# Kernel optimization log

Measured on AMD Instinct MI355X. Metric: run time of the kernel, lower is better.

Reference implementation:

```python
import jax, jax.numpy as jnp
import numpy as np

N, M, H, C = 20000, 20000, 32, 128
KP_EXTENT = 0.6
EPS = 1e-5


def _kpconv(q_pts, s_pts, neighb_inds, x, kernel_points, weights):
    """Rigid KPConv, linear influence, 'sum' aggregation, Predator-style density norm."""
    # shadow point / shadow feature padding (index M is the shadow slot)
    s_pad = jnp.concatenate([s_pts, jnp.full((1, 3), 1e6, s_pts.dtype)], axis=0)
    x_pad = jnp.concatenate([x, jnp.zeros((1, x.shape[1]), x.dtype)], axis=0)
    neighbors = s_pad[neighb_inds] - q_pts[:, None, :]              # [N,H,3]
    diff = neighbors[:, :, None, :] - kernel_points[None, None]      # [N,H,K,3]
    sq = jnp.sum(diff * diff, axis=-1)                               # [N,H,K]
    dist = jnp.sqrt(jnp.maximum(sq, 1e-12))
    all_weights = jnp.clip(1.0 - dist / KP_EXTENT, 0.0, None)        # linear KP influence
    neighb_x = x_pad[neighb_inds]                                    # [N,H,C]
    weighted = jnp.einsum('nhk,nhc->nkc', all_weights, neighb_x)     # [N,K,C]
    out = jnp.einsum('nkc,kcd->nd', weighted, weights)               # [N,D]
    # density normalization by number of valid neighbors
    feat_sum = jnp.sum(neighb_x, axis=-1)                            # [N,H]
    n_num = jnp.maximum(jnp.sum(feat_sum > 0.0, axis=-1), 1)         # [N]
    return out / n_num[:, None].astype(out.dtype)


def _segment_norm(x, len0):
    """Per-cloud (instance) normalization over stacked points, 2 clouds, no affine."""
    n = x.shape[0]
    seg = (jnp.arange(n) >= len0).astype(jnp.int32)                  # [N] in {0,1}
    onehot = jax.nn.one_hot(seg, 2, dtype=x.dtype)                   # [N,2]
    cnt = jnp.maximum(onehot.sum(axis=0), 1.0)                       # [2]
    mean = (onehot.T @ x) / cnt[:, None]                             # [2,C]
    var = (onehot.T @ (x * x)) / cnt[:, None] - mean * mean          # [2,C]
    return (x - mean[seg]) * jax.lax.rsqrt(var[seg] + EPS)


def _batchnorm1d(x, gamma, beta):
    mean = jnp.mean(x, axis=0)
    var = jnp.mean(x * x, axis=0) - mean * mean                      # biased, as torch BN
    return (x - mean) * jax.lax.rsqrt(var + EPS) * gamma + beta


def _rand_kernel_points(key, k, radius):
    pts = jax.random.normal(key, (k, 3), dtype=jnp.float32)
    pts = pts / jnp.linalg.norm(pts, axis=1, keepdims=True)
    r = jax.random.uniform(jax.random.fold_in(key, 1), (k, 1)) ** (1.0 / 3.0)
    return pts * r * radius


def setup_inputs() -> dict:
    key = jax.random.key(0)
    ks = jax.random.split(key, 10)
    D = C // 2  # 64, per-branch out channels
    q_pts = jax.random.uniform(ks[0], (N, 3), dtype=jnp.float32)
    s_pts = jax.random.uniform(ks[1], (M, 3), dtype=jnp.float32)
    neighb_inds = jax.random.randint(ks[2], (N, H), 0, M)
    x = jax.random.normal(ks[3], (M, C), dtype=jnp.float32)
    stack_lengths_post = jnp.array([N // 2, N - N // 2], dtype=jnp.int32)
    kp_mini = _rand_kernel_points(ks[4], 7, 1.0 * 1.5)               # radius * 1.5
    w_mini = jax.random.normal(ks[5], (7, C, D), dtype=jnp.float32) * (1.0 / np.sqrt(C))
    kp_mid = _rand_kernel_points(ks[6], 13, 1.0)                      # radius
    w_mid = jax.random.normal(ks[7], (13, C, D), dtype=jnp.float32) * (1.0 / np.sqrt(C))
    w_midmini = jax.random.normal(ks[8], (D, D), dtype=jnp.float32) * (1.0 / np.sqrt(D))
    w_final = jax.random.normal(ks[9], (C, C), dtype=jnp.float32) * (1.0 / np.sqrt(C))
    gamma_final = jnp.ones((C,), jnp.float32)
    beta_final = jnp.zeros((C,), jnp.float32)
    return dict(q_pts=q_pts, s_pts=s_pts, neighb_inds=neighb_inds, x=x,
                stack_lengths_post=stack_lengths_post,
                kp_mini=kp_mini, w_mini=w_mini, kp_mid=kp_mid, w_mid=w_mid,
                w_midmini=w_midmini, w_final=w_final,
                gamma_final=gamma_final, beta_final=beta_final)


def reference(q_pts, s_pts, neighb_inds, x, stack_lengths_post,
              kp_mini, w_mini, kp_mid, w_mid, w_midmini, w_final,
              gamma_final, beta_final):
    len0 = stack_lengths_post[0]
    x1 = _kpconv(q_pts, s_pts, neighb_inds, x, kp_mini, w_mini)      # [N, C//2]
    x1 = _segment_norm(x1, len0)
    x2 = _kpconv(q_pts, s_pts, neighb_inds, x, kp_mid, w_mid)        # [N, C//2]
    x2 = _segment_norm(x2, len0)
    x2 = (x1 + x2) @ w_midmini.T                                     # nn.Linear(bias=False)
    xc = jnp.concatenate([x1, x2], axis=1)                           # [N, C]
    out = xc @ w_final.T
    out = _batchnorm1d(out, gamma_final, beta_final)
    return jax.nn.relu(out)
```

## Files before the change

kernel.cpp:

```cpp
#include <hip/hip_runtime.h>
#include <math.h>

#define NQ 20000
#define MS 20000
#define HN 32
#define CH 128
#define DH 64
#define KTOT 20
#define KMINI 7
#define EPSN 1e-5f
#define NKT 80
#define KT_Y1 28

#define OFF_ROWSUM 0
#define OFF_Y1     20480
#define OFF_Y2     (OFF_Y1 + NQ*DH)
#define OFF_SEGSUM (OFF_Y2 + NQ*DH)
#define OFF_BNSUM  (OFF_SEGSUM + 512)
#define OFF_BNSQ   (OFF_BNSUM + 128)
#define OFF_OUTPRE (OFF_BNSQ + 128)
#define OFF_WSWZ   (OFF_OUTPRE + NQ*CH)
#define OFF_CFRAG  (OFF_WSWZ + 163840)
#define OFF_XBF    (OFF_CFRAG + 8192)
#define TOT_FLOATS (OFF_XBF + NQ*CH/2)

#define PK 40
#define PQ 840

typedef __attribute__((ext_vector_type(8))) short bf16x8;
typedef __attribute__((ext_vector_type(4))) float f32x4;
typedef __attribute__((ext_vector_type(4))) unsigned short us4;
typedef __attribute__((ext_vector_type(8))) unsigned short us8;

static __device__ inline unsigned short f2bf(float f) {
    unsigned int u = __float_as_uint(f);
    unsigned int r = (u + 0x7fffu + ((u >> 16) & 1u)) >> 16;
    return (unsigned short)r;
}

__global__ __launch_bounds__(256) void k_prep(
    const float* __restrict__ x, float* __restrict__ rowsum,
    const float* __restrict__ w_mini, const float* __restrict__ w_mid,
    const float* __restrict__ w_midmini, const float* __restrict__ w_final,
    unsigned short* __restrict__ wswz, unsigned short* __restrict__ cfrag,
    unsigned short* __restrict__ x_bf)
{
    const int t = threadIdx.x;
    if (blockIdx.x < 1250) {
        int row = blockIdx.x * 16 + (t >> 4);
        int l16 = t & 15;
        const float4* xr = (const float4*)&x[(size_t)row * CH + l16 * 8];
        float4 a = xr[0], b = xr[1];
        if (x_bf) {
            us8 v;
            v[0] = f2bf(a.x); v[1] = f2bf(a.y); v[2] = f2bf(a.z); v[3] = f2bf(a.w);
            v[4] = f2bf(b.x); v[5] = f2bf(b.y); v[6] = f2bf(b.z); v[7] = f2bf(b.w);
            *(us8*)&x_bf[(size_t)row * CH + l16 * 8] = v;
        }
        double s = (double)a.x + a.y + a.z + a.w + b.x + b.y + b.z + b.w;
        #pragma unroll
        for (int off = 8; off > 0; off >>= 1) s += __shfl_down(s, off, 64);
        if (l16 == 0) rowsum[row] = (float)s;
    } else if (blockIdx.x < 2530) {
        int gid = (blockIdx.x - 1250) * 256 + t;
        if (gid >= NKT * 8 * 512) return;
        int j = gid & 7;
        int l = (gid >> 3) & 63;
        int ntkt = gid >> 9;
        int nt = ntkt & 7;
        int kt = ntkt >> 3;
        int kg = kt * 32 + ((l >> 4) << 3) + j;
        int d  = nt * 16 + (l & 15);
        int k = kg >> 7, c = kg & 127;
        float v = 0.0f;
        if (k < KMINI && d < DH)        v = w_mini[((size_t)k * CH + c) * DH + d];
        else if (k >= KMINI && d >= DH) v = w_mid[((size_t)(k - KMINI) * CH + c) * DH + (d - DH)];
        wswz[gid] = f2bf(v);
    } else {
        int b2 = blockIdx.x - 2530;
        int kt = b2 >> 3, nt = b2 & 7;
        for (int e = t; e < 512; e += 256) {
            int l = e >> 3, j = e & 7;
            int i = kt * 32 + ((l >> 4) << 3) + j;
            int jcol = nt * 16 + (l & 15);
            const float* wfr = &w_final[(size_t)jcol * 128 + 64];
            int ec = i & 63;
            float dsum = 0.f;
            #pragma unroll 8
            for (int dd = 0; dd < 64; ++dd)
                dsum += w_midmini[dd * 64 + ec] * wfr[dd];
            float cv = dsum + ((i < 64) ? w_final[(size_t)jcol * 128 + i] : 0.f);
            cfrag[(size_t)(kt * 8 + nt) * 512 + e] = f2bf(cv);
        }
    }
}

__global__ __launch_bounds__(256) void k_fused2(
    const float* __restrict__ q_pts, const float* __restrict__ s_pts,
    const int* __restrict__ inds, const unsigned short* __restrict__ x_bf,
    const float* __restrict__ kp_mini, const float* __restrict__ kp_mid,
    const float* __restrict__ rowsum, const unsigned short* __restrict__ wswz,
    const int* __restrict__ stacklen,
    float* __restrict__ y1, float* __restrict__ y2, float* __restrict__ segsum)
{
    __shared__ __align__(16) char pool[36096];
    unsigned short* Pt = (unsigned short*)pool;
    unsigned short* xg = (unsigned short*)(pool + 26880);
    float* nbv = (float*)pool;
    __shared__ int nidx[512];
    __shared__ float kpts[KTOT][3];
    __shared__ int vcnt[16];
    __shared__ float winv[16];

    const int t = threadIdx.x;
    const int l = t & 63;
    const int w = t >> 6;
    const int c16 = l & 15;
    const int quad = l >> 4;
    const int n0 = blockIdx.x * 16;

    if (t < KTOT * 3) {
        int k = t / 3, j = t % 3;
        kpts[k][j] = (k < KMINI) ? kp_mini[k * 3 + j] : kp_mid[(k - KMINI) * 3 + j];
    }
    if (t < 16) vcnt[t] = 0;
    __syncthreads();

    for (int tt = t; tt < 512; tt += 256) {
        int r = tt >> 5, h = tt & 31;
        int n = n0 + r;
        int idx = inds[n * HN + h];
        nidx[tt] = idx;
        float qx = q_pts[n * 3 + 0], qy = q_pts[n * 3 + 1], qz = q_pts[n * 3 + 2];
        nbv[tt * 3 + 0] = s_pts[idx * 3 + 0] - qx;
        nbv[tt * 3 + 1] = s_pts[idx * 3 + 1] - qy;
        nbv[tt * 3 + 2] = s_pts[idx * 3 + 2] - qz;
        if (rowsum[idx] > 0.0f) atomicAdd(&vcnt[r], 1);
    }
    __syncthreads();
    if (t < 16) winv[t] = 1.0f / (float)max(vcnt[t], 1);
    __syncthreads();

    bf16x8 aw0[4], aw1[4];
    const float k0x = kpts[c16][0], k0y = kpts[c16][1], k0z = kpts[c16][2];
    const bool v1 = (c16 < 4);
    const float k1x = v1 ? kpts[16 + c16][0] : 0.f;
    const float k1y = v1 ? kpts[16 + c16][1] : 0.f;
    const float k1z = v1 ? kpts[16 + c16][2] : 0.f;
    #pragma unroll
    for (int s = 0; s < 4; ++s) {
        const int qi = w * 4 + s;
        const float wi = winv[qi];
        const float* nvb = nbv + (qi * 32 + quad * 8) * 3;
        #pragma unroll
        for (int j = 0; j < 8; ++j) {
            float bx = nvb[j * 3 + 0], by = nvb[j * 3 + 1], bz = nvb[j * 3 + 2];
            float dx = bx - k0x, dy = by - k0y, dz = bz - k0z;
            float d = sqrtf(fmaxf(dx * dx + dy * dy + dz * dz, 1e-12f));
            aw0[s][j] = (short)f2bf(fmaxf(1.0f - d * (1.0f / 0.6f), 0.0f) * wi);
            if (v1) {
                dx = bx - k1x; dy = by - k1y; dz = bz - k1z;
                d = sqrtf(fmaxf(dx * dx + dy * dy + dz * dz, 1e-12f));
                aw1[s][j] = (short)f2bf(fmaxf(1.0f - d * (1.0f / 0.6f), 0.0f) * wi);
            } else {
                aw1[s][j] = 0;
            }
        }
    }
    __syncthreads();

    f32x4 accY1 = (f32x4){0.f, 0.f, 0.f, 0.f};
    f32x4 accY2 = (f32x4){0.f, 0.f, 0.f, 0.f};
    unsigned short* xgw = xg + w * (32 * 36);
    const f32x4 zero4 = (f32x4){0.f, 0.f, 0.f, 0.f};

    for (int ktc = 0; ktc < 4; ++ktc) {
        #pragma unroll
        for (int s = 0; s < 4; ++s) {
            const int qi = w * 4 + s;
            #pragma unroll
            for (int i = 0; i < 2; ++i) {
                int gid = i * 64 + l;
                int h = gid >> 2, c8 = gid & 3;
                int idx = nidx[qi * 32 + h];
                us8 v = *(const us8*)&x_bf[(size_t)idx * CH + ktc * 32 + c8 * 8];
                us4 va = (us4){(unsigned short)v[0], (unsigned short)v[1],
                               (unsigned short)v[2], (unsigned short)v[3]};
                us4 vb = (us4){(unsigned short)v[4], (unsigned short)v[5],
                               (unsigned short)v[6], (unsigned short)v[7]};
                *(us4*)&xgw[h * 36 + c8 * 8]     = va;
                *(us4*)&xgw[h * 36 + c8 * 8 + 4] = vb;
            }
            asm volatile("s_waitcnt lgkmcnt(0)" ::: "memory");
            #pragma unroll
            for (int cf = 0; cf < 2; ++cf) {
                bf16x8 bb;
                #pragma unroll
                for (int j = 0; j < 8; ++j)
                    bb[j] = (short)xgw[(quad * 8 + j) * 36 + cf * 16 + c16];
                f32x4 d0 = __builtin_amdgcn_mfma_f32_16x16x32_bf16(aw0[s], bb, zero4, 0, 0, 0);
                f32x4 d1 = __builtin_amdgcn_mfma_f32_16x16x32_bf16(aw1[s], bb, zero4, 0, 0, 0);
                unsigned short* pq = Pt + qi * PQ + cf * 16 + c16;
                #pragma unroll
                for (int reg = 0; reg < 4; ++reg)
                    pq[(quad * 4 + reg) * PK] = f2bf(d0[reg]);
                if (quad == 0) {
                    #pragma unroll
                    for (int reg = 0; reg < 4; ++reg)
                        pq[(16 + reg) * PK] = f2bf(d1[reg]);
                }
            }
        }
        __syncthreads();

        #pragma unroll
        for (int k = 0; k < KTOT; ++k) {
            int ktg = k * 4 + ktc;
            bf16x8 a = *(const bf16x8*)&Pt[c16 * PQ + k * PK + quad * 8];
            int nt = (k < KMINI) ? w : 4 + w;
            bf16x8 b = *(const bf16x8*)&wswz[((size_t)(ktg * 8 + nt) << 9) + l * 8];
            if (k < KMINI) accY1 = __builtin_amdgcn_mfma_f32_16x16x32_bf16(a, b, accY1, 0, 0, 0);
            else           accY2 = __builtin_amdgcn_mfma_f32_16x16x32_bf16(a, b, accY2, 0, 0, 0);
        }
        __syncthreads();
    }

    const int len0 = stacklen[0];
    const bool all0 = (n0 + 15 < len0);
    const bool all1 = (n0 >= len0);
    const int ch = w * 16 + c16;
    #pragma unroll
    for (int half = 0; half < 2; ++half) {
        f32x4 acc = half ? accY2 : accY1;
        float* yb = half ? y2 : y1;
        const int sbase = half ? 256 : 0;
        float s0 = 0.f, q0 = 0.f, s1 = 0.f, q1 = 0.f;
        #pragma unroll
        for (int reg = 0; reg < 4; ++reg) {
            int row = n0 + quad * 4 + reg;
            float v = acc[reg];
            yb[(size_t)row * DH + ch] = v;
            if (row < len0) { s0 += v; q0 += v * v; }
            else            { s1 += v; q1 += v * v; }
        }
        s0 += __shfl_xor(s0, 16); s0 += __shfl_xor(s0, 32);
        q0 += __shfl_xor(q0, 16); q0 += __shfl_xor(q0, 32);
        s1 += __shfl_xor(s1, 16); s1 += __shfl_xor(s1, 32);
        q1 += __shfl_xor(q1, 16); q1 += __shfl_xor(q1, 32);
        if (quad == 0) {
            if (!all1) {
                atomicAdd(&segsum[sbase + 0 * 64 + ch], s0);
                atomicAdd(&segsum[sbase + 1 * 64 + ch], q0);
            }
            if (!all0) {
                atomicAdd(&segsum[sbase + 2 * 64 + ch], s1);
                atomicAdd(&segsum[sbase + 3 * 64 + ch], q1);
            }
        }
    }
}

__global__ __launch_bounds__(128) void k_tailmm(
    const float* __restrict__ y1, const float* __restrict__ y2,
    const float* __restrict__ segsum, const int* __restrict__ stacklen,
    const unsigned short* __restrict__ cfrag,
    float* __restrict__ outpre, float* __restrict__ bnsum, float* __restrict__ bnsq)
{
    __shared__ __align__(16) unsigned short alds[32 * 136];
    __shared__ float sstat[4][2][64];
    const int t = threadIdx.x;
    const int mb = blockIdx.x * 32;
    const int len0 = stacklen[0];

    for (int tt = t; tt < 256; tt += 128) {
        int combo = tt >> 6, ch = tt & 63;
        float cnt = (float)max((combo & 1) ? (NQ - len0) : len0, 1);
        float S = segsum[(combo * 2 + 0) * 64 + ch];
        float Q = segsum[(combo * 2 + 1) * 64 + ch];
        float mean = S / cnt;
        float var = Q / cnt - mean * mean;
        sstat[combo][0][ch] = mean;
        sstat[combo][1][ch] = rsqrtf(fmaxf(var, 0.f) + EPSN);
    }
    __syncthreads();

    for (int tt = t; tt < 32 * 32; tt += 128) {
        int r = tt >> 5, c4 = tt & 31;
        int n = mb + r;
        us4 v4 = (us4){0, 0, 0, 0};
        if (n < NQ) {
            int s = (n >= len0) ? 1 : 0;
            int c = c4 * 4;
            if (c < 64) {
                float4 yv = *(const float4*)&y1[(size_t)n * DH + c];
                v4[0] = f2bf((yv.x - sstat[s][0][c + 0]) * sstat[s][1][c + 0]);
                v4[1] = f2bf((yv.y - sstat[s][0][c + 1]) * sstat[s][1][c + 1]);
                v4[2] = f2bf((yv.z - sstat[s][0][c + 2]) * sstat[s][1][c + 2]);
                v4[3] = f2bf((yv.w - sstat[s][0][c + 3]) * sstat[s][1][c + 3]);
            } else {
                int c2 = c - 64;
                float4 yv = *(const float4*)&y2[(size_t)n * DH + c2];
                v4[0] = f2bf((yv.x - sstat[2 + s][0][c2 + 0]) * sstat[2 + s][1][c2 + 0]);
                v4[1] = f2bf((yv.y - sstat[2 + s][0][c2 + 1]) * sstat[2 + s][1][c2 + 1]);
                v4[2] = f2bf((yv.z - sstat[2 + s][0][c2 + 2]) * sstat[2 + s][1][c2 + 2]);
                v4[3] = f2bf((yv.w - sstat[2 + s][0][c2 + 3]) * sstat[2 + s][1][c2 + 3]);
            }
        }
        *(us4*)(alds + r * 136 + c4 * 4) = v4;
    }
    __syncthreads();

    const int l = t & 63, w = t >> 6;
    f32x4 acc[8];
    #pragma unroll
    for (int q = 0; q < 8; ++q) acc[q] = (f32x4){0.f, 0.f, 0.f, 0.f};

    const unsigned short* ap = alds + (w * 16 + (l & 15)) * 136 + ((l >> 4) << 3);
    const unsigned short* bp = cfrag + l * 8;
    #pragma unroll
    for (int kt = 0; kt < 4; ++kt) {
        bf16x8 a = *(const bf16x8*)(ap + kt * 32);
        #pragma unroll
        for (int nt = 0; nt < 8; ++nt) {
            bf16x8 b = *(const bf16x8*)(bp + (size_t)((kt * 8 + nt) << 9));
            acc[nt] = __builtin_amdgcn_mfma_f32_16x16x32_bf16(a, b, acc[nt], 0, 0, 0);
        }
    }

    const int quad = l >> 4, c16 = l & 15;
    #pragma unroll
    for (int nt = 0; nt < 8; ++nt) {
        float s = 0.f, q = 0.f;
        #pragma unroll
        for (int reg = 0; reg < 4; ++reg) {
            int row = mb + w * 16 + quad * 4 + reg;
            float v = acc[nt][reg];
            if (row < NQ) outpre[(size_t)row * CH + nt * 16 + c16] = v;
            else v = 0.f;
            s += v; q += v * v;
        }
        s += __shfl_xor(s, 16); s += __shfl_xor(s, 32);
        q += __shfl_xor(q, 16); q += __shfl_xor(q, 32);
        if (quad == 0) {
            atomicAdd(&bnsum[nt * 16 + c16], s);
            atomicAdd(&bnsq[nt * 16 + c16], q);
        }
    }
}

__global__ __launch_bounds__(256) void k_kpconv(
    const float* __restrict__ q_pts, const float* __restrict__ s_pts,
    const int* __restrict__ inds, const float* __restrict__ x,
    const float* __restrict__ kp_mini, const float* __restrict__ kp_mid,
    const float* __restrict__ w_mini, const float* __restrict__ w_mid,
    const float* __restrict__ rowsum,
    float* __restrict__ y1, float* __restrict__ y2)
{
    __shared__ __align__(16) float kpts[KTOT][3];
    __shared__ __align__(16) float nb[128][3];
    __shared__ int   nidx[128];
    __shared__ int   vcnt[4];
    __shared__ float winv[4];
    __shared__ __align__(16) float wts[4][HN][KTOT];
    __shared__ __align__(16) float wt[KTOT][CH][4];
    __shared__ __align__(16) float part[128][4];

    const int t = threadIdx.x;
    const int n0 = blockIdx.x * 4;

    if (t < KTOT * 3) {
        int k = t / 3, j = t % 3;
        kpts[k][j] = (k < KMINI) ? kp_mini[k * 3 + j] : kp_mid[(k - KMINI) * 3 + j];
    }
    if (t < 4) vcnt[t] = 0;
    __syncthreads();

    if (t < 128) {
        int r = t >> 5, h = t & 31;
        int n = n0 + r;
        int idx = inds[n * HN + h];
        nidx[t] = idx;
        float qx = q_pts[n * 3 + 0], qy = q_pts[n * 3 + 1], qz = q_pts[n * 3 + 2];
        nb[t][0] = s_pts[idx * 3 + 0] - qx;
        nb[t][1] = s_pts[idx * 3 + 1] - qy;
        nb[t][2] = s_pts[idx * 3 + 2] - qz;
        if (rowsum[idx] > 0.0f) atomicAdd(&vcnt[r], 1);
    }
    __syncthreads();
    if (t < 4) winv[t] = 1.0f / (float)max(vcnt[t], 1);
    __syncthreads();

    for (int tt = t; tt < 4 * HN * KTOT; tt += 256) {
        int r = tt / (HN * KTOT);
        int rem = tt % (HN * KTOT);
        int h = rem / KTOT, k = rem % KTOT;
        float dx = nb[r * HN + h][0] - kpts[k][0];
        float dy = nb[r * HN + h][1] - kpts[k][1];
        float dz = nb[r * HN + h][2] - kpts[k][2];
        float sq = dx * dx + dy * dy + dz * dz;
        float dist = sqrtf(fmaxf(sq, 1e-12f));
        float w = fmaxf(1.0f - dist * (1.0f / 0.6f), 0.0f);
        wts[r][h][k] = w * winv[r];
    }
    __syncthreads();

    {
        const int g = t >> 7;
        const int c = t & 127;
        for (int rr = 0; rr < 2; ++rr) {
            const int r = g + rr * 2;
            float acc[KTOT];
            #pragma unroll
            for (int k = 0; k < KTOT; ++k) acc[k] = 0.0f;
            for (int h = 0; h < HN; ++h) {
                int idx = nidx[r * HN + h];
                float xv = x[(size_t)idx * CH + c];
                const float4* wp = (const float4*)&wts[r][h][0];
                float4 wa = wp[0], wb = wp[1], wc = wp[2], wd = wp[3], we = wp[4];
                acc[0]  += wa.x * xv; acc[1]  += wa.y * xv; acc[2]  += wa.z * xv; acc[3]  += wa.w * xv;
                acc[4]  += wb.x * xv; acc[5]  += wb.y * xv; acc[6]  += wb.z * xv; acc[7]  += wb.w * xv;
                acc[8]  += wc.x * xv; acc[9]  += wc.y * xv; acc[10] += wc.z * xv; acc[11] += wc.w * xv;
                acc[12] += wd.x * xv; acc[13] += wd.y * xv; acc[14] += wd.z * xv; acc[15] += wd.w * xv;
                acc[16] += we.x * xv; acc[17] += we.y * xv; acc[18] += we.z * xv; acc[19] += we.w * xv;
            }
            #pragma unroll
            for (int k = 0; k < KTOT; ++k) wt[k][c][r] = acc[k];
        }
    }
    __syncthreads();

    {
        const int d = t & 127;
        const int half = t >> 7;
        const int c0 = half * 64;
        float o0 = 0.f, o1 = 0.f, o2 = 0.f, o3 = 0.f;
        if (d < DH) {
            for (int k = 0; k < KMINI; ++k) {
                const float* wp = &w_mini[((size_t)k * CH + c0) * DH + d];
                for (int c = c0; c < c0 + 64; ++c) {
                    float wv = *wp; wp += DH;
                    const float4 wtv = *(const float4*)&wt[k][c][0];
                    o0 += wv * wtv.x; o1 += wv * wtv.y; o2 += wv * wtv.z; o3 += wv * wtv.w;
                }
            }
        } else {
            const int dd = d - DH;
            for (int k = KMINI; k < KTOT; ++k) {
                const float* wp = &w_mid[((size_t)(k - KMINI) * CH + c0) * DH + dd];
                for (int c = c0; c < c0 + 64; ++c) {
                    float wv = *wp; wp += DH;
                    const float4 wtv = *(const float4*)&wt[k][c][0];
                    o0 += wv * wtv.x; o1 += wv * wtv.y; o2 += wv * wtv.z; o3 += wv * wtv.w;
                }
            }
        }
        if (half == 1) { part[d][0] = o0; part[d][1] = o1; part[d][2] = o2; part[d][3] = o3; }
        __syncthreads();
        if (half == 0) {
            o0 += part[d][0]; o1 += part[d][1]; o2 += part[d][2]; o3 += part[d][3];
            if (d < DH) {
                y1[(size_t)(n0 + 0) * DH + d] = o0;
                y1[(size_t)(n0 + 1) * DH + d] = o1;
                y1[(size_t)(n0 + 2) * DH + d] = o2;
                y1[(size_t)(n0 + 3) * DH + d] = o3;
            } else {
                const int dd = d - DH;
                y2[(size_t)(n0 + 0) * DH + dd] = o0;
                y2[(size_t)(n0 + 1) * DH + dd] = o1;
                y2[(size_t)(n0 + 2) * DH + dd] = o2;
                y2[(size_t)(n0 + 3) * DH + dd] = o3;
            }
        }
    }
}

__global__ __launch_bounds__(256) void k_segpart(
    const float* __restrict__ y1, const float* __restrict__ y2,
    const int* __restrict__ stacklen, float* __restrict__ segsum)
{
    const int t = threadIdx.x;
    const int ch = t & 63, grp = t >> 6;
    const int len0 = stacklen[0];
    float a0 = 0.f, a1 = 0.f, a2 = 0.f, a3 = 0.f;
    float b0 = 0.f, b1 = 0.f, b2 = 0.f, b3 = 0.f;
    for (int r = blockIdx.x * 4 + grp; r < NQ; r += 256 * 4) {
        float v1 = y1[(size_t)r * DH + ch];
        float v2 = y2[(size_t)r * DH + ch];
        bool in1 = (r >= len0);
        float m0 = in1 ? 0.f : 1.f, m1 = 1.f - m0;
        a0 += m0 * v1; a1 += m0 * v1 * v1; a2 += m1 * v1; a3 += m1 * v1 * v1;
        b0 += m0 * v2; b1 += m0 * v2 * v2; b2 += m1 * v2; b3 += m1 * v2 * v2;
    }
    __shared__ float red[4][8][64];
    red[grp][0][ch] = a0; red[grp][1][ch] = a1; red[grp][2][ch] = a2; red[grp][3][ch] = a3;
    red[grp][4][ch] = b0; red[grp][5][ch] = b1; red[grp][6][ch] = b2; red[grp][7][ch] = b3;
    __syncthreads();
    for (int tt = t; tt < 512; tt += 256) {
        int j = tt >> 6, c = tt & 63;
        float s = red[0][j][c] + red[1][j][c] + red[2][j][c] + red[3][j][c];
        atomicAdd(&segsum[j * 64 + c], s);
    }
}

__global__ __launch_bounds__(256) void k_tail(
    const float* __restrict__ y1, const float* __restrict__ y2,
    const float* __restrict__ segsum, const int* __restrict__ stacklen,
    const float* __restrict__ w_midmini, const float* __restrict__ w_final,
    float* __restrict__ outpre, float* __restrict__ bnsum, float* __restrict__ bnsq)
{
    __shared__ __align__(16) float sstat[4][2][64];
    __shared__ __align__(16) float sbuf[8][64];
    __shared__ __align__(16) float xc[8][128];
    __shared__ float lsum[2][128], lsq[2][128];
    const int n0 = blockIdx.x * 8;
    const int t = threadIdx.x;
    const int len0 = stacklen[0];

    {
        int combo = t >> 6, ch = t & 63;
        float cnt = (float)max((combo & 1) ? (NQ - len0) : len0, 1);
        float S = segsum[(combo * 2 + 0) * 64 + ch];
        float Q = segsum[(combo * 2 + 1) * 64 + ch];
        float mean = S / cnt;
        float var = Q / cnt - mean * mean;
        sstat[combo][0][ch] = mean;
        sstat[combo][1][ch] = rsqrtf(fmaxf(var, 0.f) + EPSN);
    }
    __syncthreads();

    for (int tt = t; tt < 8 * 64; tt += 256) {
        int r = tt >> 6, d = tt & 63;
        int n = n0 + r;
        int s = (n >= len0) ? 1 : 0;
        float x1n = (y1[(size_t)n * DH + d] - sstat[s][0][d]) * sstat[s][1][d];
        float x2n = (y2[(size_t)n * DH + d] - sstat[2 + s][0][d]) * sstat[2 + s][1][d];
        xc[r][d] = x1n;
        sbuf[r][d] = x1n + x2n;
    }
    __syncthreads();

    for (int tt = t; tt < 8 * 64; tt += 256) {
        int r = tt >> 6, d = tt & 63;
        float a = 0.f;
        const float4* wmr = (const float4*)&w_midmini[(size_t)d * 64];
        const float4* sv = (const float4*)&sbuf[r][0];
        #pragma unroll
        for (int e4 = 0; e4 < 16; ++e4) {
            float4 w4 = wmr[e4], s4 = sv[e4];
            a += w4.x * s4.x + w4.y * s4.y + w4.z * s4.z + w4.w * s4.w;
        }
        xc[r][64 + d] = a;
    }
    __syncthreads();

    {
        const int j = t & 127;
        const int g = t >> 7;
        float o0 = 0.f, o1 = 0.f, o2 = 0.f, o3 = 0.f;
        const float4* wfr = (const float4*)&w_final[(size_t)j * 128];
        #pragma unroll 8
        for (int i4 = 0; i4 < 32; ++i4) {
            float4 wf = wfr[i4];
            float4 a0 = *(const float4*)&xc[g + 0][i4 * 4];
            float4 a1 = *(const float4*)&xc[g + 2][i4 * 4];
            float4 a2 = *(const float4*)&xc[g + 4][i4 * 4];
            float4 a3 = *(const float4*)&xc[g + 6][i4 * 4];
            o0 += wf.x * a0.x + wf.y * a0.y + wf.z * a0.z + wf.w * a0.w;
            o1 += wf.x * a1.x + wf.y * a1.y + wf.z * a1.z + wf.w * a1.w;
            o2 += wf.x * a2.x + wf.y * a2.y + wf.z * a2.z + wf.w * a2.w;
            o3 += wf.x * a3.x + wf.y * a3.y + wf.z * a3.z + wf.w * a3.w;
        }
        outpre[(size_t)(n0 + g + 0) * CH + j] = o0;
        outpre[(size_t)(n0 + g + 2) * CH + j] = o1;
        outpre[(size_t)(n0 + g + 4) * CH + j] = o2;
        outpre[(size_t)(n0 + g + 6) * CH + j] = o3;
        lsum[g][j] = o0 + o1 + o2 + o3;
        lsq[g][j]  = o0 * o0 + o1 * o1 + o2 * o2 + o3 * o3;
        __syncthreads();
        if (g == 0) {
            atomicAdd(&bnsum[j], lsum[0][j] + lsum[1][j]);
            atomicAdd(&bnsq[j],  lsq[0][j] + lsq[1][j]);
        }
    }
}

__global__ __launch_bounds__(256) void k_bnapply(const float* __restrict__ outpre,
    const float* __restrict__ bnsum, const float* __restrict__ bnsq,
    const float* __restrict__ gamma, const float* __restrict__ beta,
    float* __restrict__ out)
{
    int e4 = blockIdx.x * 256 + threadIdx.x;
    if (e4 >= NQ * CH / 4) return;
    int j0 = (e4 * 4) & 127;
    float4 v = ((const float4*)outpre)[e4];
    float vv[4] = {v.x, v.y, v.z, v.w};
    float res[4];
    #pragma unroll
    for (int i = 0; i < 4; ++i) {
        int j = j0 + i;
        float mean = bnsum[j] * (1.0f / NQ);
        float var = bnsq[j] * (1.0f / NQ) - mean * mean;
        float rstd = rsqrtf(fmaxf(var, 0.f) + EPSN);
        float r = (vv[i] - mean) * rstd * gamma[j] + beta[j];
        res[i] = fmaxf(r, 0.f);
    }
    ((float4*)out)[e4] = make_float4(res[0], res[1], res[2], res[3]);
}

extern "C" void kernel_launch(void* const* d_in, const int* in_sizes, int n_in,
                              void* d_out, int out_size, void* d_ws, size_t ws_size,
                              hipStream_t stream) {
    const float* q_pts     = (const float*)d_in[0];
    const float* s_pts     = (const float*)d_in[1];
    const int*   inds      = (const int*)d_in[2];
    const float* x         = (const float*)d_in[3];
    const int*   stacklen  = (const int*)d_in[4];
    const float* kp_mini   = (const float*)d_in[5];
    const float* w_mini    = (const float*)d_in[6];
    const float* kp_mid    = (const float*)d_in[7];
    const float* w_mid     = (const float*)d_in[8];
    const float* w_midmini = (const float*)d_in[9];
    const float* w_final   = (const float*)d_in[10];
    const float* gamma     = (const float*)d_in[11];
    const float* beta      = (const float*)d_in[12];

    float* ws      = (float*)d_ws;
    float* rowsum  = ws + OFF_ROWSUM;
    float* y1      = ws + OFF_Y1;
    float* y2      = ws + OFF_Y2;
    float* segsum  = ws + OFF_SEGSUM;
    float* bnsum   = ws + OFF_BNSUM;
    float* bnsq    = ws + OFF_BNSQ;
    float* outpre  = ws + OFF_OUTPRE;
    unsigned short* wswz  = (unsigned short*)(ws + OFF_WSWZ);
    unsigned short* cfrag = (unsigned short*)(ws + OFF_CFRAG);
    unsigned short* x_bf  = (unsigned short*)(ws + OFF_XBF);

    hipMemsetAsync(segsum, 0, 768 * sizeof(float), stream);

    if (ws_size >= (size_t)TOT_FLOATS * sizeof(float)) {
        k_prep<<<1250 + 1280 + 32, 256, 0, stream>>>(x, rowsum, w_mini, w_mid,
                                                     w_midmini, w_final, wswz, cfrag, x_bf);
        k_fused2<<<NQ / 16, 256, 0, stream>>>(q_pts, s_pts, inds, x_bf, kp_mini, kp_mid,
                                              rowsum, wswz, stacklen, y1, y2, segsum);
        k_tailmm<<<(NQ + 31) / 32, 128, 0, stream>>>(y1, y2, segsum, stacklen, cfrag,
                                                     outpre, bnsum, bnsq);
    } else {
        k_prep<<<1250, 256, 0, stream>>>(x, rowsum, w_mini, w_mid,
                                         w_midmini, w_final, wswz, cfrag, (unsigned short*)0);
        k_kpconv<<<NQ / 4, 256, 0, stream>>>(q_pts, s_pts, inds, x, kp_mini, kp_mid,
                                             w_mini, w_mid, rowsum, y1, y2);
        k_segpart<<<256, 256, 0, stream>>>(y1, y2, stacklen, segsum);
        k_tail<<<NQ / 8, 256, 0, stream>>>(y1, y2, segsum, stacklen, w_midmini, w_final,
                                           outpre, bnsum, bnsq);
    }

    k_bnapply<<<(NQ * CH / 4 + 255) / 256, 256, 0, stream>>>(outpre, bnsum, bnsq,
                                                             gamma, beta, (float*)d_out);
}
```

Baseline: 230.8 us.

## Prefetch next gathered x rows into registers and stage weight-fold operands in LDS

In the fused KPConv kernel, the gathered neighbour feature loads for the next (ktc, s) step are now issued one iteration ahead into registers. The row pointers are precomputed once from nidx. This hides global gather latency behind the MFMA work of the current step. The cfrag precompute blocks also stage w_midmini and the w_final slices in shared memory instead of re-reading them from global memory inside the inner loop. The cost is more registers (eight pointers plus two prefetch buffers), which may lower occupancy.

```diff
diff --git a/kernel.cpp b/kernel.cpp
--- a/kernel.cpp
+++ b/kernel.cpp
@@ -77,19 +77,32 @@
         else if (k >= KMINI && d >= DH) v = w_mid[((size_t)(k - KMINI) * CH + c) * DH + (d - DH)];
         wswz[gid] = f2bf(v);
     } else {
+        __shared__ float wm[4096];
+        __shared__ float wfs[16][64];
+        __shared__ float wfd[16][32];
         int b2 = blockIdx.x - 2530;
         int kt = b2 >> 3, nt = b2 & 7;
+        for (int e = t; e < 4096; e += 256) wm[e] = w_midmini[e];
+        for (int e = t; e < 1024; e += 256) {
+            int r = e >> 6, dd = e & 63;
+            wfs[r][dd] = w_final[(size_t)(nt * 16 + r) * 128 + 64 + dd];
+        }
+        for (int e = t; e < 512; e += 256) {
+            int r = e >> 5, i2 = e & 31;
+            int col = kt * 32 + i2;
+            wfd[r][i2] = (col < 64) ? w_final[(size_t)(nt * 16 + r) * 128 + col] : 0.f;
+        }
+        __syncthreads();
         for (int e = t; e < 512; e += 256) {
             int l = e >> 3, j = e & 7;
             int i = kt * 32 + ((l >> 4) << 3) + j;
-            int jcol = nt * 16 + (l & 15);
-            const float* wfr = &w_final[(size_t)jcol * 128 + 64];
+            int r = l & 15;
             int ec = i & 63;
             float dsum = 0.f;
             #pragma unroll 8
             for (int dd = 0; dd < 64; ++dd)
-                dsum += w_midmini[dd * 64 + ec] * wfr[dd];
-            float cv = dsum + ((i < 64) ? w_final[(size_t)jcol * 128 + i] : 0.f);
+                dsum += wm[dd * 64 + ec] * wfs[r][dd];
+            float cv = dsum + ((i < 64) ? wfd[r][i - kt * 32] : 0.f);
             cfrag[(size_t)(kt * 8 + nt) * 512 + e] = f2bf(cv);
         }
     }
@@ -167,6 +180,17 @@
             }
         }
     }
+
+    const int hA = l >> 2, c8 = l & 3;
+    const int hB = 16 + hA;
+    const unsigned short* pA[4];
+    const unsigned short* pB[4];
+    #pragma unroll
+    for (int s = 0; s < 4; ++s) {
+        int qi = w * 4 + s;
+        pA[s] = x_bf + (size_t)nidx[qi * 32 + hA] * CH + c8 * 8;
+        pB[s] = x_bf + (size_t)nidx[qi * 32 + hB] * CH + c8 * 8;
+    }
     __syncthreads();
 
     f32x4 accY1 = (f32x4){0.f, 0.f, 0.f, 0.f};
@@ -174,22 +198,32 @@
     unsigned short* xgw = xg + w * (32 * 36);
     const f32x4 zero4 = (f32x4){0.f, 0.f, 0.f, 0.f};
 
+    us8 pfA = *(const us8*)(pA[0]);
+    us8 pfB = *(const us8*)(pB[0]);
+
     for (int ktc = 0; ktc < 4; ++ktc) {
         #pragma unroll
         for (int s = 0; s < 4; ++s) {
             const int qi = w * 4 + s;
-            #pragma unroll
-            for (int i = 0; i < 2; ++i) {
-                int gid = i * 64 + l;
-                int h = gid >> 2, c8 = gid & 3;
-                int idx = nidx[qi * 32 + h];
-                us8 v = *(const us8*)&x_bf[(size_t)idx * CH + ktc * 32 + c8 * 8];
-                us4 va = (us4){(unsigned short)v[0], (unsigned short)v[1],
-                               (unsigned short)v[2], (unsigned short)v[3]};
-                us4 vb = (us4){(unsigned short)v[4], (unsigned short)v[5],
-                               (unsigned short)v[6], (unsigned short)v[7]};
-                *(us4*)&xgw[h * 36 + c8 * 8]     = va;
-                *(us4*)&xgw[h * 36 + c8 * 8 + 4] = vb;
+            {
+                us4 va = (us4){(unsigned short)pfA[0], (unsigned short)pfA[1],
+                               (unsigned short)pfA[2], (unsigned short)pfA[3]};
+                us4 vb = (us4){(unsigned short)pfA[4], (unsigned short)pfA[5],
+                               (unsigned short)pfA[6], (unsigned short)pfA[7]};
+                *(us4*)&xgw[hA * 36 + c8 * 8]     = va;
+                *(us4*)&xgw[hA * 36 + c8 * 8 + 4] = vb;
+                us4 vc = (us4){(unsigned short)pfB[0], (unsigned short)pfB[1],
+                               (unsigned short)pfB[2], (unsigned short)pfB[3]};
+                us4 vd = (us4){(unsigned short)pfB[4], (unsigned short)pfB[5],
+                               (unsigned short)pfB[6], (unsigned short)pfB[7]};
+                *(us4*)&xgw[hB * 36 + c8 * 8]     = vc;
+                *(us4*)&xgw[hB * 36 + c8 * 8 + 4] = vd;
+            }
+            const int nit = ktc * 4 + s + 1;
+            if (nit < 16) {
+                const int nktc = nit >> 2, ns = nit & 3;
+                pfA = *(const us8*)(pA[ns] + nktc * 32);
+                pfB = *(const us8*)(pB[ns] + nktc * 32);
             }
             asm volatile("s_waitcnt lgkmcnt(0)" ::: "memory");
             #pragma unroll
```

Measured after the change: 248.1 us. 1.07x slower.
